# Kernel tuning notes

Hardware: AMD Instinct MI355X
Metric: run time of the kernel (lower is better)

Reference implementation:

```python
import jax, jax.numpy as jnp
import numpy as np

EPS = 1e-8


def setup_inputs() -> dict:
    key = jax.random.key(0)
    k1, k2 = jax.random.split(key)
    x = jax.random.normal(k1, (32, 16, 4096), dtype=jnp.float32)
    # shapelets param: (in_channels, num_shapelets, shapelets_size)
    shapelets = jax.random.normal(k2, (16, 64, 64), dtype=jnp.float32)
    return {"x": x, "shapelets": shapelets}


def reference(x, shapelets):
    # x: (B, C, L); shapelets: (C, K, S)
    S = shapelets.shape[2]
    C = x.shape[1]
    W = x.shape[2] - S + 1
    # sliding windows, equivalent to torch unfold(2, S, 1): (B, C, W, S)
    idx = jnp.arange(W)[:, None] + jnp.arange(S)[None, :]
    win = x[:, :, idx]
    win = win / jnp.maximum(jnp.linalg.norm(win, axis=3, keepdims=True), EPS)
    sh = shapelets / jnp.maximum(jnp.linalg.norm(shapelets, axis=2, keepdims=True), EPS)
    # pairwise cosine dot, then mean over channels: (B, W, K)
    sim = jnp.einsum('bcws,cks->bwk', win, sh) / C
    # relu then global max over window positions; torch keeps the summed dim -> (B, 1, K)
    out = jnp.max(jax.nn.relu(sim), axis=1)[:, None, :]
    return out
```

## Files before the change

### kernel.cpp

```cpp
#include <hip/hip_runtime.h>

typedef unsigned int u32;
typedef unsigned short u16;
typedef __bf16 bf16x8 __attribute__((ext_vector_type(8)));
typedef float f32x4 __attribute__((ext_vector_type(4)));

static __device__ __forceinline__ u16 f2bf(float f) {
  u32 u = __float_as_uint(f);
  return (u16)((u + 0x7fffu + ((u >> 16) & 1u)) >> 16);
}
static __device__ __forceinline__ float b2f(u16 v) {
  return __uint_as_float(((u32)v) << 16);
}
static __device__ __forceinline__ u32 pk2(u16 lo, u16 hi) {
  return (u32)lo | ((u32)hi << 16);
}

__global__ __launch_bounds__(256) void prep_kernel(const float* __restrict__ sh,
                                                   u16* __restrict__ shn2,
                                                   float* __restrict__ out) {
  const int c = blockIdx.x;
  if (c == 0) {
    float4 z = {0.f, 0.f, 0.f, 0.f};
    *(float4*)&out[threadIdx.x * 8] = z;
    *(float4*)&out[threadIdx.x * 8 + 4] = z;
  }
  const int s = threadIdx.x & 63;
  const int kw = threadIdx.x >> 6;
  for (int k = kw; k < 64; k += 4) {
    float v = sh[(c * 64 + k) * 64 + s];
    float ss = v * v;
#pragma unroll
    for (int o = 1; o < 64; o <<= 1) ss += __shfl_xor(ss, o, 64);
    float iw = 1.0f / fmaxf(sqrtf(ss), 1e-8f);
    const int chunk = c * 8 + (k >> 4) * 2 + (s >> 5);
    const int pos = ((k & 15) + (((s & 31) >> 3) << 4)) * 8 + (s & 7);
    shn2[chunk * 512 + pos] = f2bf(v * iw);
  }
}

#define WT 256
#define CSTRIDE 168
#define SSTRIDE 2728

__global__ __launch_bounds__(512, 2) void main_kernel(const float* __restrict__ x,
                                                      const u16* __restrict__ shn2,
                                                      float* __restrict__ out) {
  __shared__ u32 xs[4 * SSTRIDE];
  __shared__ u16 invwb[16 * WT];
  __shared__ int redbuf[64];

  const int tid = threadIdx.x;
  const int lane = tid & 63;
  const int wid = tid >> 6;
  const int w0 = blockIdx.x * WT;
  const int b = blockIdx.y;
  const float* xb = x + (size_t)b * 16 * 4096;

  if (tid < 64) redbuf[tid] = 0;

  {
    const int q = tid & 31;
    const int c = tid >> 5;
    if (q < 20) {
      const float* xc = xb + c * 4096;
      const int e0 = w0 + 16 * q;
      float xv[20];
      if (e0 + 19 < 4096) {
#pragma unroll
        for (int r = 0; r < 5; ++r) *(float4*)&xv[4 * r] = *(const float4*)&xc[e0 + 4 * r];
      } else {
#pragma unroll
        for (int j = 0; j < 20; ++j) {
          int g = e0 + j;
          xv[j] = xc[g < 4096 ? g : 4095];
        }
      }
      u16 bf[20];
#pragma unroll
      for (int j = 0; j < 20; ++j) bf[j] = f2bf(xv[j]);
#pragma unroll
      for (int s = 0; s < 4; ++s) {
        u32 pk[8];
#pragma unroll
        for (int r = 0; r < 8; ++r) pk[r] = pk2(bf[2 * r + s], bf[2 * r + s + 1]);
        u32* dst = &xs[s * SSTRIDE + c * CSTRIDE + 8 * q];
        *(uint4*)dst = make_uint4(pk[0], pk[1], pk[2], pk[3]);
        *(uint4*)(dst + 4) = make_uint4(pk[4], pk[5], pk[6], pk[7]);
      }
    }
  }

  {
    const int c = tid >> 5;
    const int wb = (tid & 31) * 8;
    const float* xc = xb + c * 4096;
    const int e0 = w0 + wb;
    float hd[8], tl[8], ss = 0.f;
    if (e0 + 71 < 4096) {
#pragma unroll
      for (int r = 0; r < 16; ++r) {
        float4 v = *(const float4*)&xc[e0 + 4 * r];
        if (r < 2) {
          hd[4 * r + 0] = v.x; hd[4 * r + 1] = v.y;
          hd[4 * r + 2] = v.z; hd[4 * r + 3] = v.w;
        }
        ss += v.x * v.x + v.y * v.y + v.z * v.z + v.w * v.w;
      }
#pragma unroll
      for (int r = 0; r < 2; ++r) {
        float4 v = *(const float4*)&xc[e0 + 64 + 4 * r];
        tl[4 * r + 0] = v.x; tl[4 * r + 1] = v.y;
        tl[4 * r + 2] = v.z; tl[4 * r + 3] = v.w;
      }
    } else {
#pragma unroll
      for (int j = 0; j < 72; ++j) {
        int g = e0 + j;
        float v = xc[g < 4096 ? g : 4095];
        if (j < 8) hd[j] = v;
        if (j >= 64) tl[j - 64] = v;
        if (j < 64) ss += v * v;
      }
    }
    u16 ov[8];
#pragma unroll
    for (int i = 0; i < 8; ++i) {
      float iw = 0.0625f / fmaxf(sqrtf(fmaxf(ss, 0.f)), 1e-8f);
      ov[i] = (e0 + i < 4033) ? f2bf(iw) : (u16)0;
      ss += tl[i] * tl[i] - hd[i] * hd[i];
    }
    *(uint4*)&invwb[c * WT + wb] = make_uint4(pk2(ov[0], ov[1]), pk2(ov[2], ov[3]),
                                              pk2(ov[4], ov[5]), pk2(ov[6], ov[7]));
  }

  __syncthreads();

  f32x4 acc[2][4];
#pragma unroll
  for (int mt = 0; mt < 2; ++mt)
#pragma unroll
    for (int nt = 0; nt < 4; ++nt) acc[mt][nt] = (f32x4){0.f, 0.f, 0.f, 0.f};

  const int m = lane & 15;
  const int h = lane >> 4;
  const u32* xbase = xs + (m & 3) * SSTRIDE;
  const int joff = 16 * wid + 2 * (m >> 2) + 4 * h;
  const u16* shb = shn2 + lane * 8;
  const int iwoff = 32 * wid + 4 * h;

#pragma unroll 2
  for (int c = 0; c < 16; ++c) {
    const u32* xc = xbase + c * CSTRIDE;
    bf16x8 af[4];
#pragma unroll
    for (int f = 0; f < 4; ++f) {
      const u32* p = xc + joff + 8 * f;
      uint2 lo = *(const uint2*)p;
      uint2 hi = *(const uint2*)(p + 2);
      af[f] = __builtin_bit_cast(bf16x8, make_uint4(lo.x, lo.y, hi.x, hi.y));
    }
    const u16* sc = shb + c * 4096;
    bf16x8 bfr[4][2];
#pragma unroll
    for (int nt = 0; nt < 4; ++nt)
#pragma unroll
      for (int ks = 0; ks < 2; ++ks)
        bfr[nt][ks] = __builtin_bit_cast(bf16x8, *(const uint4*)(sc + (nt * 2 + ks) * 512));

#pragma unroll
    for (int mt = 0; mt < 2; ++mt) {
      ushort4 r4 = *(const ushort4*)&invwb[c * WT + iwoff + 16 * mt];
      f32x4 iw = {b2f(r4.x), b2f(r4.y), b2f(r4.z), b2f(r4.w)};
#pragma unroll
      for (int nt = 0; nt < 4; ++nt) {
        f32x4 d = {0.f, 0.f, 0.f, 0.f};
        d = __builtin_amdgcn_mfma_f32_16x16x32_bf16(af[mt],     bfr[nt][0], d, 0, 0, 0);
        d = __builtin_amdgcn_mfma_f32_16x16x32_bf16(af[mt + 2], bfr[nt][1], d, 0, 0, 0);
        acc[mt][nt] += iw * d;
      }
    }
  }

#pragma unroll
  for (int nt = 0; nt < 4; ++nt) {
    float v = 0.f;
#pragma unroll
    for (int mt = 0; mt < 2; ++mt)
      v = fmaxf(v, fmaxf(fmaxf(acc[mt][nt].x, acc[mt][nt].y),
                         fmaxf(acc[mt][nt].z, acc[mt][nt].w)));
    v = fmaxf(v, __shfl_xor(v, 16, 64));
    v = fmaxf(v, __shfl_xor(v, 32, 64));
    if (lane < 16) atomicMax(&redbuf[nt * 16 + lane], __float_as_int(v));
  }
  __syncthreads();
  if (tid < 64) atomicMax((int*)&out[b * 64 + tid], redbuf[tid]);
}

extern "C" void kernel_launch(void* const* d_in, const int* in_sizes, int n_in,
                              void* d_out, int out_size, void* d_ws, size_t ws_size,
                              hipStream_t stream) {
  const float* x = (const float*)d_in[0];
  const float* sh = (const float*)d_in[1];
  float* out = (float*)d_out;
  u16* shn2 = (u16*)d_ws;

  prep_kernel<<<dim3(16), dim3(256), 0, stream>>>(sh, shn2, out);
  main_kernel<<<dim3(16, 32), dim3(512), 0, stream>>>(x, shn2, out);
}
```

Measured before the change: 41.89 us.

## Retile waves to 64 windows x 32 shapelets, keep fp32 norms, widen prep grid

Each wave now covers 64 window positions and 32 shapelets instead of 32 windows and all 64 shapelets. This halves the per-wave global loads of shapelet B fragments and raises A-fragment reuse from LDS, at the cost of two more A fragments per channel. The inverse window norms are now kept in LDS as fp32, which drops the bf16 rounding and unpack work but doubles that buffer's LDS footprint. The prep kernel is spread over 64 blocks instead of 16 so more of the GPU is used for shapelet normalization.

```diff
diff --git a/kernel.cpp b/kernel.cpp
--- a/kernel.cpp
+++ b/kernel.cpp
@@ -9,9 +9,6 @@
   u32 u = __float_as_uint(f);
   return (u16)((u + 0x7fffu + ((u >> 16) & 1u)) >> 16);
 }
-static __device__ __forceinline__ float b2f(u16 v) {
-  return __uint_as_float(((u32)v) << 16);
-}
 static __device__ __forceinline__ u32 pk2(u16 lo, u16 hi) {
   return (u32)lo | ((u32)hi << 16);
 }
@@ -19,20 +16,23 @@
 __global__ __launch_bounds__(256) void prep_kernel(const float* __restrict__ sh,
                                                    u16* __restrict__ shn2,
                                                    float* __restrict__ out) {
-  const int c = blockIdx.x;
-  if (c == 0) {
+  if (blockIdx.x == 0) {
     float4 z = {0.f, 0.f, 0.f, 0.f};
     *(float4*)&out[threadIdx.x * 8] = z;
     *(float4*)&out[threadIdx.x * 8 + 4] = z;
   }
   const int s = threadIdx.x & 63;
-  const int kw = threadIdx.x >> 6;
-  for (int k = kw; k < 64; k += 4) {
-    float v = sh[(c * 64 + k) * 64 + s];
+  const int wv = threadIdx.x >> 6;
+  const int row0 = blockIdx.x * 16 + wv * 4;
+#pragma unroll
+  for (int r = 0; r < 4; ++r) {
+    const int row = row0 + r;
+    float v = sh[row * 64 + s];
     float ss = v * v;
 #pragma unroll
     for (int o = 1; o < 64; o <<= 1) ss += __shfl_xor(ss, o, 64);
     float iw = 1.0f / fmaxf(sqrtf(ss), 1e-8f);
+    const int c = row >> 6, k = row & 63;
     const int chunk = c * 8 + (k >> 4) * 2 + (s >> 5);
     const int pos = ((k & 15) + (((s & 31) >> 3) << 4)) * 8 + (s & 7);
     shn2[chunk * 512 + pos] = f2bf(v * iw);
@@ -47,7 +47,7 @@
                                                       const u16* __restrict__ shn2,
                                                       float* __restrict__ out) {
   __shared__ u32 xs[4 * SSTRIDE];
-  __shared__ u16 invwb[16 * WT];
+  __shared__ float invwb[16 * WT];
   __shared__ int redbuf[64];
 
   const int tid = threadIdx.x;
@@ -123,57 +123,58 @@
         if (j < 64) ss += v * v;
       }
     }
-    u16 ov[8];
+    float ov[8];
 #pragma unroll
     for (int i = 0; i < 8; ++i) {
       float iw = 0.0625f / fmaxf(sqrtf(fmaxf(ss, 0.f)), 1e-8f);
-      ov[i] = (e0 + i < 4033) ? f2bf(iw) : (u16)0;
+      ov[i] = (e0 + i < 4033) ? iw : 0.f;
       ss += tl[i] * tl[i] - hd[i] * hd[i];
     }
-    *(uint4*)&invwb[c * WT + wb] = make_uint4(pk2(ov[0], ov[1]), pk2(ov[2], ov[3]),
-                                              pk2(ov[4], ov[5]), pk2(ov[6], ov[7]));
+    *(float4*)&invwb[c * WT + wb] = make_float4(ov[0], ov[1], ov[2], ov[3]);
+    *(float4*)&invwb[c * WT + wb + 4] = make_float4(ov[4], ov[5], ov[6], ov[7]);
   }
 
   __syncthreads();
 
-  f32x4 acc[2][4];
-#pragma unroll
-  for (int mt = 0; mt < 2; ++mt)
-#pragma unroll
-    for (int nt = 0; nt < 4; ++nt) acc[mt][nt] = (f32x4){0.f, 0.f, 0.f, 0.f};
+  f32x4 acc[4][2];
+#pragma unroll
+  for (int mt = 0; mt < 4; ++mt)
+#pragma unroll
+    for (int nt = 0; nt < 2; ++nt) acc[mt][nt] = (f32x4){0.f, 0.f, 0.f, 0.f};
 
   const int m = lane & 15;
   const int h = lane >> 4;
+  const int wgrp = wid >> 1;
+  const int kgrp = wid & 1;
   const u32* xbase = xs + (m & 3) * SSTRIDE;
-  const int joff = 16 * wid + 2 * (m >> 2) + 4 * h;
-  const u16* shb = shn2 + lane * 8;
-  const int iwoff = 32 * wid + 4 * h;
+  const int joff = 32 * wgrp + 2 * (m >> 2) + 4 * h;
+  const u16* shb = shn2 + lane * 8 + kgrp * 4 * 512;
+  const int iwbase = 64 * wgrp + 4 * h;
 
 #pragma unroll 2
   for (int c = 0; c < 16; ++c) {
     const u32* xc = xbase + c * CSTRIDE;
-    bf16x8 af[4];
-#pragma unroll
-    for (int f = 0; f < 4; ++f) {
+    bf16x8 af[6];
+#pragma unroll
+    for (int f = 0; f < 6; ++f) {
       const u32* p = xc + joff + 8 * f;
       uint2 lo = *(const uint2*)p;
       uint2 hi = *(const uint2*)(p + 2);
       af[f] = __builtin_bit_cast(bf16x8, make_uint4(lo.x, lo.y, hi.x, hi.y));
     }
     const u16* sc = shb + c * 4096;
-    bf16x8 bfr[4][2];
-#pragma unroll
-    for (int nt = 0; nt < 4; ++nt)
+    bf16x8 bfr[2][2];
+#pragma unroll
+    for (int nt = 0; nt < 2; ++nt)
 #pragma unroll
       for (int ks = 0; ks < 2; ++ks)
         bfr[nt][ks] = __builtin_bit_cast(bf16x8, *(const uint4*)(sc + (nt * 2 + ks) * 512));
 
 #pragma unroll
-    for (int mt = 0; mt < 2; ++mt) {
-      ushort4 r4 = *(const ushort4*)&invwb[c * WT + iwoff + 16 * mt];
-      f32x4 iw = {b2f(r4.x), b2f(r4.y), b2f(r4.z), b2f(r4.w)};
-#pragma unroll
-      for (int nt = 0; nt < 4; ++nt) {
+    for (int mt = 0; mt < 4; ++mt) {
+      f32x4 iw = *(const f32x4*)&invwb[c * WT + iwbase + 16 * mt];
+#pragma unroll
+      for (int nt = 0; nt < 2; ++nt) {
         f32x4 d = {0.f, 0.f, 0.f, 0.f};
         d = __builtin_amdgcn_mfma_f32_16x16x32_bf16(af[mt],     bfr[nt][0], d, 0, 0, 0);
         d = __builtin_amdgcn_mfma_f32_16x16x32_bf16(af[mt + 2], bfr[nt][1], d, 0, 0, 0);
@@ -183,15 +184,15 @@
   }
 
 #pragma unroll
-  for (int nt = 0; nt < 4; ++nt) {
+  for (int nt = 0; nt < 2; ++nt) {
     float v = 0.f;
 #pragma unroll
-    for (int mt = 0; mt < 2; ++mt)
+    for (int mt = 0; mt < 4; ++mt)
       v = fmaxf(v, fmaxf(fmaxf(acc[mt][nt].x, acc[mt][nt].y),
                          fmaxf(acc[mt][nt].z, acc[mt][nt].w)));
     v = fmaxf(v, __shfl_xor(v, 16, 64));
     v = fmaxf(v, __shfl_xor(v, 32, 64));
-    if (lane < 16) atomicMax(&redbuf[nt * 16 + lane], __float_as_int(v));
+    if (lane < 16) atomicMax(&redbuf[kgrp * 32 + nt * 16 + lane], __float_as_int(v));
   }
   __syncthreads();
   if (tid < 64) atomicMax((int*)&out[b * 64 + tid], redbuf[tid]);
@@ -205,6 +206,6 @@
   float* out = (float*)d_out;
   u16* shn2 = (u16*)d_ws;
 
-  prep_kernel<<<dim3(16), dim3(256), 0, stream>>>(sh, shn2, out);
+  prep_kernel<<<dim3(64), dim3(256), 0, stream>>>(sh, shn2, out);
   main_kernel<<<dim3(16, 32), dim3(512), 0, stream>>>(x, shn2, out);
 }
```

After: 37.18 us. -11.2%, faster.
